# Kernel tuning notes

Measured on AMD Instinct MI355X. Metric: run time of the kernel, lower is better.

## Reference

```python
import jax, jax.numpy as jnp
import numpy as np

HEADS = 16
DIM_HEAD = 64
SCALE = DIM_HEAD ** -0.5
CMEM_RATIO = 4
MEM_LEN = 1024
CMEM_LEN = 256


def shift(x):
    # relative-position shift trick; x: [b, h, i, j]
    b, h, i, j = x.shape
    x = jnp.concatenate([x, jnp.zeros((b, h, i, i), x.dtype)], axis=-1)
    l = i + j - 1
    x = x.reshape(b, h, -1)
    pad = (-x.shape[-1]) % l
    x = jnp.concatenate([x, jnp.zeros((b, h, pad), x.dtype)], axis=-1).reshape(b, h, -1, l)
    return x[..., :i, i - 1:]


def setup_inputs() -> dict:
    key = jax.random.key(0)
    ks = jax.random.split(key, 8)
    b, t, e = 2, 1024, 1024
    kv_len = CMEM_LEN + MEM_LEN + t
    inp = {}
    inp['x'] = jax.random.normal(ks[0], (b, t, e), jnp.float32)
    inp['mem'] = jax.random.normal(ks[1], (b, MEM_LEN, e), jnp.float32)
    inp['cmem'] = jax.random.normal(ks[2], (b, CMEM_LEN, e), jnp.float32)
    inp['pos_emb'] = jax.random.normal(ks[3], (HEADS, kv_len, DIM_HEAD), jnp.float32)
    inp['input_mask'] = jnp.ones((b, t), bool)
    inp['Wq'] = jax.random.normal(ks[4], (e, e), jnp.float32) * 0.02
    inp['Wkv'] = jax.random.normal(ks[5], (e, 2 * e), jnp.float32) * 0.02
    inp['Wo'] = jax.random.normal(ks[6], (e, e), jnp.float32) * 0.02
    inp['bo'] = jnp.zeros((e,), jnp.float32)
    inp['conv_w'] = jax.random.normal(ks[7], (e, e, CMEM_RATIO), jnp.float32) * 0.02
    inp['conv_b'] = jnp.zeros((e,), jnp.float32)
    return inp


def _attend(x, mem, cmem, pos_emb, input_mask, Wq, Wkv):
    b, t, e = x.shape
    mem_len, cmem_len = mem.shape[1], cmem.shape[1]
    q = x @ Wq
    kv_input = jnp.concatenate([cmem, mem, x], axis=1)
    kv_len = kv_input.shape[1]
    k, v = jnp.split(kv_input @ Wkv, 2, axis=-1)
    mh = lambda z: z.reshape(b, -1, HEADS, DIM_HEAD).transpose(0, 2, 1, 3)  # [b,h,s,d]
    q, k, v = mh(q), mh(k), mh(v)
    dots = jnp.einsum('bhid,bhjd->bhij', q, k) * SCALE
    mask_value = -jnp.finfo(dots.dtype).max
    pe = pos_emb[:, -kv_len:].astype(q.dtype)
    pos_dots = jnp.einsum('bhid,hjd->bhij', q, pe) * SCALE
    dots = dots + shift(pos_dots)
    # padding mask (NOTE: replicates source: memory region is padded with False)
    pad_mask = input_mask[:, None, :, None] & input_mask[:, None, None, :]
    pad_mask = jnp.pad(pad_mask, ((0, 0), (0, 0), (0, 0), (mem_len + cmem_len, 0)), constant_values=False)
    dots = jnp.where(pad_mask, dots, mask_value)
    # causal mask exactly as in source (triu with diagonal=1+kv_len)
    causal = jnp.triu(jnp.ones((t, kv_len), bool), k=1 + kv_len)
    dots = jnp.where(causal[None, None], mask_value, dots)
    attn = jax.nn.softmax(dots, axis=-1)
    out = jnp.einsum('bhij,bhjd->bhid', attn, v)
    return out.transpose(0, 2, 1, 3).reshape(b, t, e)


def reference(x, mem, cmem, pos_emb, input_mask, Wq, Wkv, Wo, bo, conv_w, conv_b):
    b, t, e = x.shape
    out = _attend(x, mem, cmem, pos_emb, input_mask, Wq, Wkv)
    logits = out @ Wo + bo
    # memory update (eval mode, seq_len == t, calc_memory=True)
    cat_mem = jnp.concatenate([mem, x], axis=1)
    old_mem, new_mem = cat_mem[:, :-MEM_LEN], cat_mem[:, -MEM_LEN:]
    pad = old_mem.shape[1] % CMEM_RATIO
    if pad != 0:
        old_mem = jnp.pad(old_mem, ((0, 0), (pad, 0), (0, 0)))
    cm = jax.lax.conv_general_dilated(old_mem.transpose(0, 2, 1), conv_w, (CMEM_RATIO,), 'VALID',
                                      dimension_numbers=('NCH', 'OIH', 'NCH'))
    compressed = (cm + conv_b[None, :, None]).transpose(0, 2, 1)
    new_cmem = jnp.concatenate([cmem, compressed], axis=1)[:, -CMEM_LEN:]
    aux_loss = jnp.zeros((1,), x.dtype)
    return logits, new_mem, new_cmem, aux_loss
```

## Files before the change

### kernel.cpp

```cpp
#include <hip/hip_runtime.h>
#include <hip/hip_bf16.h>

typedef __bf16 bf16x8 __attribute__((ext_vector_type(8)));
typedef float f32x4 __attribute__((ext_vector_type(4)));

#define SCALE 0.125f
#define MFMA16 __builtin_amdgcn_mfma_f32_16x16x32_bf16

typedef __attribute__((address_space(1))) const unsigned int gas_u32;
typedef __attribute__((address_space(3))) unsigned int las_u32;

__device__ __forceinline__ void gload16(const void* g, void* l) {
  __builtin_amdgcn_global_load_lds((gas_u32*)g, (las_u32*)l, 16, 0, 0);
}

__device__ __forceinline__ unsigned short f2bf(float f) {
  unsigned int u = __float_as_uint(f);
  u = (u + 0x7fffu + ((u >> 16) & 1u)) >> 16;
  return (unsigned short)u;
}
__device__ __forceinline__ f32x4 f4zero() {
  f32x4 v; v[0] = 0.f; v[1] = 0.f; v[2] = 0.f; v[3] = 0.f; return v;
}
__device__ __forceinline__ bf16x8 ld8(const unsigned short* p) {
  return *(const bf16x8*)p;
}

__global__ void prep_all(const float* __restrict__ x, const float* __restrict__ mem,
                         const float* __restrict__ pe,
                         const float* __restrict__ Wq, const float* __restrict__ Wkv,
                         const float* __restrict__ Wo, const float* __restrict__ cw,
                         unsigned short* __restrict__ xb, unsigned short* __restrict__ memb,
                         float* __restrict__ newmem, float* __restrict__ aux,
                         unsigned short* __restrict__ peb,
                         unsigned short* __restrict__ WbT, unsigned short* __restrict__ WoT,
                         unsigned short* __restrict__ BcT) {
  __shared__ float tile[64][65];
  int bx = blockIdx.x;
  int tid = threadIdx.x;
  if (bx < 4096) {
    long i = (long)bx * 256 + tid;
    if (i < 524288) {
      float4 v = ((const float4*)x)[i];
      ((float4*)newmem)[i] = v;
      ushort4 o; o.x = f2bf(v.x); o.y = f2bf(v.y); o.z = f2bf(v.z); o.w = f2bf(v.w);
      ((ushort4*)xb)[i] = o;
      if (i == 0) aux[0] = 0.f;
    } else {
      long j = i - 524288;
      float4 v = ((const float4*)mem)[j];
      ushort4 o; o.x = f2bf(v.x); o.y = f2bf(v.y); o.z = f2bf(v.z); o.w = f2bf(v.w);
      ((ushort4*)memb)[j] = o;
    }
  } else if (bx < 5120) {
    long i = (long)(bx - 4096) * 256 + tid;
    int h = (int)(i >> 14);
    int rem = (int)(i & 16383);
    const float4* src = (const float4*)(pe + ((long)h * 2304 + 1280) * 64);
    float4 v = src[rem];
    ushort4 o; o.x = f2bf(v.x); o.y = f2bf(v.y); o.z = f2bf(v.z); o.w = f2bf(v.w);
    *(ushort4*)(peb + (long)h * 65536 + (long)rem * 4) = o;
  } else if (bx < 9216) {
    long i = (long)(bx - 5120) * 256 + tid;
    int o = (int)(i >> 10), ii = (int)(i & 1023);
    float4 v = *(const float4*)&cw[i * 4];
    unsigned short* base = BcT + (long)o * 4096 + ii;
    base[0]    = f2bf(v.x);
    base[1024] = f2bf(v.y);
    base[2048] = f2bf(v.z);
    base[3072] = f2bf(v.w);
  } else {
    int t = bx - 9216;
    int bxt = t & 63, byt = t >> 6;
    const float* in; unsigned short* outp; int N, bxl;
    if (bxt < 16)      { in = Wq;  outp = WbT;           N = 1024; bxl = bxt; }
    else if (bxt < 48) { in = Wkv; outp = WbT + 1048576; N = 2048; bxl = bxt - 16; }
    else               { in = Wo;  outp = WoT;           N = 1024; bxl = bxt - 48; }
    int k0 = byt * 64, n0 = bxl * 64;
    int c = tid & 63, r4 = tid >> 6;
    for (int rr = r4; rr < 64; rr += 4)
      tile[rr][c] = in[(long)(k0 + rr) * N + n0 + c];
    __syncthreads();
    for (int rr = r4; rr < 64; rr += 4)
      outp[(long)(n0 + rr) * 1024 + k0 + c] = f2bf(tile[c][rr]);
  }
}

__global__ void vt_prep(const unsigned short* __restrict__ qkvb, unsigned short* __restrict__ Vt) {
  __shared__ unsigned short L[64][72];
  int tt = blockIdx.x, h = blockIdx.y, b = blockIdx.z;
  int t0 = tt * 64;
  int tid = threadIdx.x;
  int row = tid >> 2, ch = tid & 3;
  const unsigned short* src = qkvb + (long)(b * 1024 + t0 + row) * 3072 + 2048 + h * 64;
  *(uint4*)&L[row][ch * 8]       = *(const uint4*)&src[ch * 8];
  *(uint4*)&L[row][(ch + 4) * 8] = *(const uint4*)&src[(ch + 4) * 8];
  __syncthreads();
  int d = tid >> 2, tch = tid & 3;
  unsigned short* dst = Vt + ((long)((b * 16 + h) * 64 + d)) * 1024 + t0;
  for (int s = tch; s < 8; s += 4) {
    unsigned short tmp[8];
    for (int i = 0; i < 8; ++i) tmp[i] = L[s * 8 + i][d];
    *(uint4*)&dst[s * 8] = *(const uint4*)tmp;
  }
}

__global__ void splitk_reduce_bias(const float* __restrict__ part,
                                   const float* __restrict__ bias,
                                   float* __restrict__ out) {
  int i = blockIdx.x * 256 + threadIdx.x;
  float4 a = ((const float4*)part)[i];
  for (int s = 1; s < 8; ++s) {
    float4 b = ((const float4*)(part + (long)s * 524288))[i];
    a.x += b.x; a.y += b.y; a.z += b.z; a.w += b.w;
  }
  float4 bb = *(const float4*)&bias[(i * 4) & 1023];
  a.x += bb.x; a.y += bb.y; a.z += bb.z; a.w += bb.w;
  ((float4*)out)[i] = a;
}

template<int M_REP, bool OUT_F32, bool HAS_BIAS>
__global__ __launch_bounds__(256) void gemm_bt(
    const unsigned short* __restrict__ A, const unsigned short* __restrict__ BT,
    void* __restrict__ Cout, const float* __restrict__ bias,
    int K, int lda, int ldbt, int ldc,
    int zInner, long sAo, long sAi, long sBo, long sBi, long sCo, long sCi) {
  constexpr int BM = 32 * M_REP;
  constexpr int ACH = BM / 16;
  constexpr int ABUF = BM * 32;
  __shared__ unsigned short As[2 * ABUF];
  __shared__ unsigned short Bs[2 * 4096];
  int z = blockIdx.z;
  int zo = z / zInner, zi = z % zInner;
  A += zo * sAo + zi * sAi;
  BT += zo * sBo + zi * sBi;
  long coff = zo * sCo + zi * sCi;
  int r0 = blockIdx.y * BM;
  int c0 = blockIdx.x * 128;
  int tid = threadIdx.x;
  int lane = tid & 63, wid = tid >> 6;
  int wm = wid >> 1, wn = wid & 1;
  int lr = lane & 15, lg = lane >> 4;
  int srow = lane >> 2;
  int sg8 = (((lane & 3) ^ ((lane >> 3) & 3)) * 8);

  auto stage = [&](int kt, int buf) {
    for (int c = wid; c < ACH + 8; c += 4) {
      if (c < ACH) {
        gload16(&A[(long)(r0 + c * 16 + srow) * lda + kt * 32 + sg8],
                As + buf * ABUF + c * 512);
      } else {
        int cb = c - ACH;
        gload16(&BT[(long)(c0 + cb * 16 + srow) * ldbt + kt * 32 + sg8],
                Bs + buf * 4096 + cb * 512);
      }
    }
  };

  f32x4 acc[M_REP][4];
  #pragma unroll
  for (int mi = 0; mi < M_REP; ++mi)
    #pragma unroll
    for (int nj = 0; nj < 4; ++nj) acc[mi][nj] = f4zero();

  int nK = K >> 5;
  stage(0, 0);
  asm volatile("s_waitcnt vmcnt(0)" ::: "memory");
  __syncthreads();
  for (int kt = 0; kt < nK; ++kt) {
    int cur = kt & 1;
    if (kt + 1 < nK) stage(kt + 1, cur ^ 1);
    bf16x8 af[M_REP], bfr[4];
    #pragma unroll
    for (int mi = 0; mi < M_REP; ++mi) {
      int row = wm * (16 * M_REP) + mi * 16 + lr;
      af[mi] = ld8(&As[cur * ABUF + row * 32 + ((lg ^ ((row >> 1) & 3)) * 8)]);
    }
    #pragma unroll
    for (int nj = 0; nj < 4; ++nj) {
      int row = wn * 64 + nj * 16 + lr;
      bfr[nj] = ld8(&Bs[cur * 4096 + row * 32 + ((lg ^ ((row >> 1) & 3)) * 8)]);
    }
    #pragma unroll
    for (int mi = 0; mi < M_REP; ++mi)
      #pragma unroll
      for (int nj = 0; nj < 4; ++nj)
        acc[mi][nj] = MFMA16(af[mi], bfr[nj], acc[mi][nj], 0, 0, 0);
    if (kt + 1 < nK) {
      asm volatile("s_waitcnt vmcnt(0)" ::: "memory");
      __syncthreads();
    }
  }
  float* Cf = (float*)Cout;
  unsigned short* Cb = (unsigned short*)Cout;
  #pragma unroll
  for (int mi = 0; mi < M_REP; ++mi)
    #pragma unroll
    for (int nj = 0; nj < 4; ++nj)
      #pragma unroll
      for (int j = 0; j < 4; ++j) {
        int r = r0 + wm * (16 * M_REP) + mi * 16 + lg * 4 + j;
        int c = c0 + wn * 64 + nj * 16 + lr;
        float v = acc[mi][nj][j];
        if (HAS_BIAS) v += bias[c];
        long off = coff + (long)r * ldc + c;
        if (OUT_F32) Cf[off] = v; else Cb[off] = f2bf(v);
      }
}

__global__ __launch_bounds__(256) void attn_kernel(
    const unsigned short* __restrict__ qkv,
    const unsigned short* __restrict__ Vt,
    const unsigned short* __restrict__ peb,
    unsigned short* __restrict__ obf) {
  int bid = blockIdx.x;
  int sw = ((bid & 7) << 6) | (bid >> 3);
  int rt = sw & 15, h = (sw >> 4) & 15, b = sw >> 8;
  int tid = threadIdx.x;
  int lane = tid & 63, w = tid >> 6;
  int lr = lane & 15, lg = lane >> 4;
  int r0 = rt * 64;

  __shared__ unsigned short Ks[2 * 4096];
  __shared__ unsigned short Vs[2 * 4096];
  __shared__ unsigned short PEs[3 * 4096];
  __shared__ unsigned short Ps[4][16][72];

  bf16x8 aq0, aq1;
  {
    const unsigned short* qrow = qkv + ((long)(b * 1024 + r0 + w * 16 + lr)) * 3072 + h * 64;
    aq0 = ld8(qrow + lg * 8);
    aq1 = ld8(qrow + 32 + lg * 8);
  }
  float m[4], lsum[4];
  f32x4 acc_o[4], accp[5];
  #pragma unroll
  for (int j = 0; j < 4; ++j) { m[j] = -1e30f; lsum[j] = 0.f; }
  #pragma unroll
  for (int n = 0; n < 4; ++n) acc_o[n] = f4zero();

  const unsigned short* kbase = qkv + (long)b * 3145728 + 1024 + h * 64;
  const unsigned short* vtb = Vt + ((long)(b * 16 + h)) * 65536;
  const unsigned short* peh = peb + (long)h * 65536;
  int rg = r0 + w * 16 + lg * 4;
  int qq = w * 16 + lg * 4;

  int srow = (lane >> 3) & 7;
  int sslot = lane & 7;

  auto stageKV = [&](int kt, int buf) {
    int c0 = kt * 64;
    #pragma unroll
    for (int i = 0; i < 2; ++i) {
      int chunk = w * 2 + i;
      int row = chunk * 8 + srow;
      int g = sslot ^ (row & 7);
      gload16(&kbase[(long)(c0 + row) * 3072 + g * 8], Ks + buf * 4096 + chunk * 512);
      gload16(&vtb[(long)row * 1024 + c0 + g * 8], Vs + buf * 4096 + chunk * 512);
    }
  };
  auto stagePE = [&](int blk) {
    int slot = blk % 3;
    #pragma unroll
    for (int i = 0; i < 2; ++i) {
      int chunk = w * 2 + i;
      int row = chunk * 8 + srow;
      int u = min(blk * 64 + row, 1023);
      int g = sslot ^ (row & 7);
      gload16(&peh[(long)u * 64 + g * 8], PEs + slot * 4096 + chunk * 512);
    }
  };
  auto peMFMA = [&](int pl, int ub) -> f32x4 {
    int u = min(ub + 48 - w * 16 + pl * 16 + lr, 1023);
    int off = ((u >> 6) % 3) * 4096 + (u & 63) * 64;
    bf16x8 p0 = ld8(&PEs[off + ((lg ^ (u & 7)) * 8)]);
    bf16x8 p1 = ld8(&PEs[off + (((4 + lg) ^ (u & 7)) * 8)]);
    f32x4 r = f4zero();
    r = MFMA16(aq0, p0, r, 0, 0, 0);
    r = MFMA16(aq1, p1, r, 0, 0, 0);
    return r;
  };

  stageKV(0, 0);
  stagePE(15 - rt);
  stagePE(16 - rt);
  asm volatile("s_waitcnt vmcnt(0)" ::: "memory");
  __syncthreads();

  for (int kt = 0; kt < 16; ++kt) {
    int cur = kt & 1;
    bool band = (kt <= rt);
    int ub = 960 + (kt - rt) * 64;
    if (kt < 15) stageKV(kt + 1, cur ^ 1);
    if (kt + 1 <= rt) stagePE(17 + kt - rt);
    f32x4 accs[4];
    #pragma unroll
    for (int nj = 0; nj < 4; ++nj) {
      int row = nj * 16 + lr;
      const unsigned short* kb = &Ks[cur * 4096 + row * 64];
      bf16x8 bk0 = ld8(&kb[(lg ^ (row & 7)) * 8]);
      bf16x8 bk1 = ld8(&kb[((4 + lg) ^ (row & 7)) * 8]);
      accs[nj] = f4zero();
      accs[nj] = MFMA16(aq0, bk0, accs[nj], 0, 0, 0);
      accs[nj] = MFMA16(aq1, bk1, accs[nj], 0, 0, 0);
    }
    float qpv[4][4];
    if (band) {
      if (kt == 0) {
        #pragma unroll
        for (int pl = 0; pl < 5; ++pl) accp[pl] = peMFMA(pl, ub);
      } else {
        #pragma unroll
        for (int pl = 1; pl < 5; ++pl) accp[pl] = peMFMA(pl, ub);
      }
      #pragma unroll
      for (int j = 0; j < 4; ++j) {
        int sl = (lane & 48) | ((lr - lg * 4 - j - 1) & 15);
        bool hi = lr > lg * 4 + j;
        #pragma unroll
        for (int nj = 0; nj < 4; ++nj) {
          float vlo = __shfl(accp[nj][j], sl, 64);
          float vhi = __shfl(accp[nj + 1][j], sl, 64);
          float v = hi ? vhi : vlo;
          if (kt == rt) {
            int uu = nj * 16 + lr + 63 - (qq + j);
            if (uu > 63) v = 0.f;
          }
          qpv[nj][j] = v;
        }
      }
      accp[0] = accp[4];
    }
    float sv[4][4];
    float tmax[4] = {-1e30f, -1e30f, -1e30f, -1e30f};
    #pragma unroll
    for (int nj = 0; nj < 4; ++nj)
      #pragma unroll
      for (int j = 0; j < 4; ++j) {
        float s = accs[nj][j];
        if (band) s += qpv[nj][j];
        s *= SCALE;
        sv[nj][j] = s;
        tmax[j] = fmaxf(tmax[j], s);
      }
    for (int d = 1; d < 16; d <<= 1)
      #pragma unroll
      for (int j = 0; j < 4; ++j) tmax[j] = fmaxf(tmax[j], __shfl_xor(tmax[j], d, 64));
    float sc[4], rsum[4];
    #pragma unroll
    for (int j = 0; j < 4; ++j) {
      float mn = fmaxf(m[j], tmax[j]);
      sc[j] = __expf(m[j] - mn);
      m[j] = mn;
      rsum[j] = 0.f;
    }
    #pragma unroll
    for (int nj = 0; nj < 4; ++nj)
      #pragma unroll
      for (int j = 0; j < 4; ++j) {
        float p = __expf(sv[nj][j] - m[j]);
        rsum[j] += p;
        Ps[w][lg * 4 + j][nj * 16 + lr] = f2bf(p);
      }
    for (int d = 1; d < 16; d <<= 1)
      #pragma unroll
      for (int j = 0; j < 4; ++j) rsum[j] += __shfl_xor(rsum[j], d, 64);
    #pragma unroll
    for (int j = 0; j < 4; ++j) lsum[j] = lsum[j] * sc[j] + rsum[j];
    #pragma unroll
    for (int n = 0; n < 4; ++n)
      #pragma unroll
      for (int j = 0; j < 4; ++j) acc_o[n][j] *= sc[j];
    asm volatile("s_waitcnt lgkmcnt(0)" ::: "memory");
    __builtin_amdgcn_sched_barrier(0);
    #pragma unroll
    for (int ks = 0; ks < 2; ++ks) {
      bf16x8 ap = ld8(&Ps[w][lr][ks * 32 + lg * 8]);
      #pragma unroll
      for (int n = 0; n < 4; ++n) {
        int row = n * 16 + lr;
        bf16x8 bv = ld8(&Vs[cur * 4096 + row * 64 + (((ks * 4 + lg) ^ (row & 7)) * 8)]);
        acc_o[n] = MFMA16(ap, bv, acc_o[n], 0, 0, 0);
      }
    }
    if (kt < 15) {
      asm volatile("s_waitcnt vmcnt(0)" ::: "memory");
      __syncthreads();
    }
  }
  #pragma unroll
  for (int n = 0; n < 4; ++n)
    #pragma unroll
    for (int j = 0; j < 4; ++j) {
      float v = acc_o[n][j] / lsum[j];
      obf[((long)(b * 1024 + rg + j)) * 1024 + h * 64 + n * 16 + lr] = f2bf(v);
    }
}

extern "C" void kernel_launch(void* const* d_in, const int* in_sizes, int n_in,
                              void* d_out, int out_size, void* d_ws, size_t ws_size,
                              hipStream_t stream) {
  const float* x       = (const float*)d_in[0];
  const float* mem     = (const float*)d_in[1];
  const float* pos_emb = (const float*)d_in[3];
  const float* Wq      = (const float*)d_in[5];
  const float* Wkv     = (const float*)d_in[6];
  const float* Wo      = (const float*)d_in[7];
  const float* bo      = (const float*)d_in[8];
  const float* conv_w  = (const float*)d_in[9];
  const float* conv_b  = (const float*)d_in[10];
  float* out = (float*)d_out;

  char* ws = (char*)d_ws;
  unsigned short* xb   = (unsigned short*)(ws + 0);
  unsigned short* Vt   = xb;
  unsigned short* WbT  = (unsigned short*)(ws + 4194304);
  unsigned short* qkvb = (unsigned short*)(ws + 10485760);
  unsigned short* peb  = (unsigned short*)(ws + 23068672);
  unsigned short* obf  = (unsigned short*)(ws + 25165824);
  unsigned short* WoT  = (unsigned short*)(ws + 29360128);
  unsigned short* memb = (unsigned short*)(ws + 31457280);
  unsigned short* BcT  = (unsigned short*)(ws + 35651584);
  float* convpart = (float*)(ws + 44040192);

  float* logits   = out;
  float* new_mem  = out + 2097152;
  float* new_cmem = out + 4194304;
  float* aux      = out + 4718592;

  prep_all<<<10240, 256, 0, stream>>>(x, mem, pos_emb, Wq, Wkv, Wo, conv_w,
                                      xb, memb, new_mem, aux, peb, WbT, WoT, BcT);

  gemm_bt<2, false, false><<<dim3(24, 32, 1), 256, 0, stream>>>(
      xb, WbT, qkvb, nullptr, 1024, 1024, 1024, 3072, 1, 0, 0, 0, 0, 0, 0);

  vt_prep<<<dim3(16, 16, 2), 256, 0, stream>>>(qkvb, Vt);

  attn_kernel<<<dim3(512, 1, 1), 256, 0, stream>>>(qkvb, Vt, peb, obf);

  gemm_bt<2, true, true><<<dim3(8, 32, 1), 256, 0, stream>>>(
      obf, WoT, logits, bo, 1024, 1024, 1024, 1024, 1, 0, 0, 0, 0, 0, 0);

  gemm_bt<2, true, false><<<dim3(8, 8, 8), 256, 0, stream>>>(
      memb, BcT, convpart, nullptr, 512, 4096, 4096, 1024,
      1, 512, 0, 512, 0, 524288, 0);
  splitk_reduce_bias<<<512, 256, 0, stream>>>(convpart, conv_b, new_cmem);
}
```

Before: 242.5 us.

## Retile GEMMs, split-K output projection, drop PE LDS staging, add MFMA priority

Several changes land together. The GEMMs move to M_REP=4 (128-row tiles). The output projection becomes a 2-way split-K whose reduction is fused with the conv reduction in one kernel. The attention kernel stops staging positional embeddings in LDS and reads them straight from global memory. s_setprio raises wave priority around the MFMA blocks. The goals are better reuse per tile, more parallelism for the Wo GEMM and lower LDS pressure, at the cost of extra partial-sum traffic and uncoalesced global PE loads.

```diff
diff --git a/kernel.cpp b/kernel.cpp
--- a/kernel.cpp
+++ b/kernel.cpp
@@ -105,18 +105,28 @@
   }
 }
 
-__global__ void splitk_reduce_bias(const float* __restrict__ part,
-                                   const float* __restrict__ bias,
-                                   float* __restrict__ out) {
-  int i = blockIdx.x * 256 + threadIdx.x;
-  float4 a = ((const float4*)part)[i];
-  for (int s = 1; s < 8; ++s) {
-    float4 b = ((const float4*)(part + (long)s * 524288))[i];
-    a.x += b.x; a.y += b.y; a.z += b.z; a.w += b.w;
-  }
-  float4 bb = *(const float4*)&bias[(i * 4) & 1023];
-  a.x += bb.x; a.y += bb.y; a.z += bb.z; a.w += bb.w;
-  ((float4*)out)[i] = a;
+__global__ void reduce_both(const float* __restrict__ lpart, const float* __restrict__ bo,
+                            const float* __restrict__ cpart, const float* __restrict__ cbias,
+                            float* __restrict__ logits, float* __restrict__ cmem) {
+  int bx = blockIdx.x, tid = threadIdx.x;
+  if (bx < 2048) {
+    int i = bx * 256 + tid;
+    float4 a = ((const float4*)lpart)[i];
+    float4 b = ((const float4*)(lpart + 2097152))[i];
+    float4 bb = *(const float4*)&bo[(i * 4) & 1023];
+    a.x += b.x + bb.x; a.y += b.y + bb.y; a.z += b.z + bb.z; a.w += b.w + bb.w;
+    ((float4*)logits)[i] = a;
+  } else {
+    int i = (bx - 2048) * 256 + tid;
+    float4 a = ((const float4*)cpart)[i];
+    for (int s = 1; s < 8; ++s) {
+      float4 b = ((const float4*)(cpart + (long)s * 524288))[i];
+      a.x += b.x; a.y += b.y; a.z += b.z; a.w += b.w;
+    }
+    float4 bb = *(const float4*)&cbias[(i * 4) & 1023];
+    a.x += bb.x; a.y += bb.y; a.z += bb.z; a.w += bb.w;
+    ((float4*)cmem)[i] = a;
+  }
 }
 
 template<int M_REP, bool OUT_F32, bool HAS_BIAS>
@@ -181,11 +191,13 @@
       int row = wn * 64 + nj * 16 + lr;
       bfr[nj] = ld8(&Bs[cur * 4096 + row * 32 + ((lg ^ ((row >> 1) & 3)) * 8)]);
     }
+    __builtin_amdgcn_s_setprio(1);
     #pragma unroll
     for (int mi = 0; mi < M_REP; ++mi)
       #pragma unroll
       for (int nj = 0; nj < 4; ++nj)
         acc[mi][nj] = MFMA16(af[mi], bfr[nj], acc[mi][nj], 0, 0, 0);
+    __builtin_amdgcn_s_setprio(0);
     if (kt + 1 < nK) {
       asm volatile("s_waitcnt vmcnt(0)" ::: "memory");
       __syncthreads();
@@ -223,7 +235,6 @@
 
   __shared__ unsigned short Ks[2 * 4096];
   __shared__ unsigned short Vs[2 * 4096];
-  __shared__ unsigned short PEs[3 * 4096];
   __shared__ unsigned short Ps[4][16][72];
 
   bf16x8 aq0, aq1;
@@ -259,22 +270,11 @@
       gload16(&vtb[(long)row * 1024 + c0 + g * 8], Vs + buf * 4096 + chunk * 512);
     }
   };
-  auto stagePE = [&](int blk) {
-    int slot = blk % 3;
-    #pragma unroll
-    for (int i = 0; i < 2; ++i) {
-      int chunk = w * 2 + i;
-      int row = chunk * 8 + srow;
-      int u = min(blk * 64 + row, 1023);
-      int g = sslot ^ (row & 7);
-      gload16(&peh[(long)u * 64 + g * 8], PEs + slot * 4096 + chunk * 512);
-    }
-  };
   auto peMFMA = [&](int pl, int ub) -> f32x4 {
     int u = min(ub + 48 - w * 16 + pl * 16 + lr, 1023);
-    int off = ((u >> 6) % 3) * 4096 + (u & 63) * 64;
-    bf16x8 p0 = ld8(&PEs[off + ((lg ^ (u & 7)) * 8)]);
-    bf16x8 p1 = ld8(&PEs[off + (((4 + lg) ^ (u & 7)) * 8)]);
+    const unsigned short* pr = peh + (long)u * 64;
+    bf16x8 p0 = ld8(pr + lg * 8);
+    bf16x8 p1 = ld8(pr + 32 + lg * 8);
     f32x4 r = f4zero();
     r = MFMA16(aq0, p0, r, 0, 0, 0);
     r = MFMA16(aq1, p1, r, 0, 0, 0);
@@ -282,8 +282,6 @@
   };
 
   stageKV(0, 0);
-  stagePE(15 - rt);
-  stagePE(16 - rt);
   asm volatile("s_waitcnt vmcnt(0)" ::: "memory");
   __syncthreads();
 
@@ -292,8 +290,8 @@
     bool band = (kt <= rt);
     int ub = 960 + (kt - rt) * 64;
     if (kt < 15) stageKV(kt + 1, cur ^ 1);
-    if (kt + 1 <= rt) stagePE(17 + kt - rt);
     f32x4 accs[4];
+    __builtin_amdgcn_s_setprio(1);
     #pragma unroll
     for (int nj = 0; nj < 4; ++nj) {
       int row = nj * 16 + lr;
@@ -304,6 +302,7 @@
       accs[nj] = MFMA16(aq0, bk0, accs[nj], 0, 0, 0);
       accs[nj] = MFMA16(aq1, bk1, accs[nj], 0, 0, 0);
     }
+    __builtin_amdgcn_s_setprio(0);
     float qpv[4][4];
     if (band) {
       if (kt == 0) {
@@ -373,6 +372,7 @@
       for (int j = 0; j < 4; ++j) acc_o[n][j] *= sc[j];
     asm volatile("s_waitcnt lgkmcnt(0)" ::: "memory");
     __builtin_amdgcn_sched_barrier(0);
+    __builtin_amdgcn_s_setprio(1);
     #pragma unroll
     for (int ks = 0; ks < 2; ++ks) {
       bf16x8 ap = ld8(&Ps[w][lr][ks * 32 + lg * 8]);
@@ -383,6 +383,7 @@
         acc_o[n] = MFMA16(ap, bv, acc_o[n], 0, 0, 0);
       }
     }
+    __builtin_amdgcn_s_setprio(0);
     if (kt < 15) {
       asm volatile("s_waitcnt vmcnt(0)" ::: "memory");
       __syncthreads();
@@ -422,6 +423,7 @@
   unsigned short* memb = (unsigned short*)(ws + 31457280);
   unsigned short* BcT  = (unsigned short*)(ws + 35651584);
   float* convpart = (float*)(ws + 44040192);
+  float* lpart    = (float*)(ws + 60817408);
 
   float* logits   = out;
   float* new_mem  = out + 2097152;
@@ -431,18 +433,20 @@
   prep_all<<<10240, 256, 0, stream>>>(x, mem, pos_emb, Wq, Wkv, Wo, conv_w,
                                       xb, memb, new_mem, aux, peb, WbT, WoT, BcT);
 
-  gemm_bt<2, false, false><<<dim3(24, 32, 1), 256, 0, stream>>>(
+  gemm_bt<4, false, false><<<dim3(24, 16, 1), 256, 0, stream>>>(
       xb, WbT, qkvb, nullptr, 1024, 1024, 1024, 3072, 1, 0, 0, 0, 0, 0, 0);
 
   vt_prep<<<dim3(16, 16, 2), 256, 0, stream>>>(qkvb, Vt);
 
   attn_kernel<<<dim3(512, 1, 1), 256, 0, stream>>>(qkvb, Vt, peb, obf);
 
-  gemm_bt<2, true, true><<<dim3(8, 32, 1), 256, 0, stream>>>(
-      obf, WoT, logits, bo, 1024, 1024, 1024, 1024, 1, 0, 0, 0, 0, 0, 0);
-
-  gemm_bt<2, true, false><<<dim3(8, 8, 8), 256, 0, stream>>>(
+  gemm_bt<4, true, false><<<dim3(8, 16, 2), 256, 0, stream>>>(
+      obf, WoT, lpart, nullptr, 512, 1024, 1024, 1024,
+      1, 512, 0, 512, 0, 2097152, 0);
+
+  gemm_bt<4, true, false><<<dim3(8, 4, 8), 256, 0, stream>>>(
       memb, BcT, convpart, nullptr, 512, 4096, 4096, 1024,
       1, 512, 0, 512, 0, 524288, 0);
-  splitk_reduce_bias<<<512, 256, 0, stream>>>(convpart, conv_b, new_cmem);
-}
+
+  reduce_both<<<2560, 256, 0, stream>>>(lpart, bo, convpart, conv_b, logits, new_cmem);
+}
```

Result: slower. 249.5 us (+2.9%).
